# Performance work log

Hardware: AMD Instinct MI355X
Metric: run time of the kernel (lower is better)

The kernel has to match this reference:

```python
import jax, jax.numpy as jnp
import numpy as np
from jax import lax

L, B, D = 512, 128, 512   # listener frames, batch, listener feature dim
T, E, C, H, V = 200, 384, 128, 512, 46  # decode steps, embed, context, hidden(=E+C), vocab


def setup_inputs() -> dict:
    key = jax.random.key(0)
    ks = jax.random.split(key, 32)
    def p(i, shape, s=0.02):
        return jax.random.normal(ks[i], shape, dtype=jnp.float32) * s
    return {
        "listener_features": jax.random.normal(ks[0], (L, B, D), dtype=jnp.float32),
        "utterance_lengths": jax.random.randint(ks[1], (B,), L // 2, L + 1),
        "transcript": jax.random.randint(ks[2], (T, B), 0, V),
        "embedding": p(3, (V, E), 1.0),
        "w_ih0": p(4, (4 * H, E + C)), "w_hh0": p(5, (4 * H, H)),
        "b_ih0": jnp.zeros((4 * H,), jnp.float32), "b_hh0": jnp.zeros((4 * H,), jnp.float32),
        "w_ih1": p(6, (4 * H, H)), "w_hh1": p(7, (4 * H, H)),
        "b_ih1": jnp.zeros((4 * H,), jnp.float32), "b_hh1": jnp.zeros((4 * H,), jnp.float32),
        "w_ih2": p(8, (4 * H, H)), "w_hh2": p(9, (4 * H, H)),
        "b_ih2": jnp.zeros((4 * H,), jnp.float32), "b_hh2": jnp.zeros((4 * H,), jnp.float32),
        "phi_w": p(10, (C, H)), "phi_b": jnp.zeros((C,), jnp.float32),
        "key_w": p(11, (C, D)), "key_b": jnp.zeros((C,), jnp.float32),
        "value_w": p(12, (C, D)), "value_b": jnp.zeros((C,), jnp.float32),
        "out_w": p(13, (V, H + C)), "out_b": jnp.zeros((V,), jnp.float32),
        "init_hx0": jnp.zeros((1, H), jnp.float32), "init_cx0": jnp.zeros((1, H), jnp.float32),
        "init_hx1": jnp.zeros((1, H), jnp.float32), "init_cx1": jnp.zeros((1, H), jnp.float32),
        "init_hx2": jnp.zeros((1, H), jnp.float32), "init_cx2": jnp.zeros((1, H), jnp.float32),
    }


def _lstm_cell(x, h, c, w_ih, w_hh, b_ih, b_hh):
    gates = x @ w_ih.T + b_ih + h @ w_hh.T + b_hh  # [B,4H]
    i, f, g, o = jnp.split(gates, 4, axis=-1)
    c2 = jax.nn.sigmoid(f) * c + jax.nn.sigmoid(i) * jnp.tanh(g)
    h2 = jax.nn.sigmoid(o) * jnp.tanh(c2)
    return h2, c2


def reference(listener_features, utterance_lengths, transcript, embedding,
              w_ih0, w_hh0, b_ih0, b_hh0, w_ih1, w_hh1, b_ih1, b_hh1,
              w_ih2, w_hh2, b_ih2, b_hh2, phi_w, phi_b, key_w, key_b,
              value_w, value_b, out_w, out_b,
              init_hx0, init_cx0, init_hx1, init_cx1, init_hx2, init_cx2):
    nL, nB = listener_features.shape[0], listener_features.shape[1]
    mask = (jnp.arange(nL)[None, :] < utterance_lengths[:, None]).astype(jnp.float32)  # [B,L]
    # key/value projections are step-invariant (original recomputes them each step; same math)
    keyf = jnp.einsum('lbd,cd->blc', listener_features, key_w) + key_b   # [B,L,C]
    valf = jnp.einsum('lbd,cd->blc', listener_features, value_w) + value_b  # [B,L,C]

    def attend(hx2):
        q = hx2 @ phi_w.T + phi_b                      # [B,C]
        energy = jnp.einsum('bc,blc->bl', q, keyf)     # [B,L]
        a = jax.nn.softmax(energy, axis=-1) * mask
        a = a / jnp.maximum(jnp.sum(a, axis=-1, keepdims=True), 1e-12)  # F.normalize(p=1)
        ctx = jnp.einsum('bl,blc->bc', a, valf)        # [B,C]
        return a, ctx

    hx0 = jnp.broadcast_to(init_hx0, (nB, H)); cx0 = jnp.broadcast_to(init_cx0, (nB, H))
    hx1 = jnp.broadcast_to(init_hx1, (nB, H)); cx1 = jnp.broadcast_to(init_cx1, (nB, H))
    hx2 = jnp.broadcast_to(init_hx2, (nB, H)); cx2 = jnp.broadcast_to(init_cx2, (nB, H))
    _, ctx = attend(hx2)  # initial context from initial decoder state

    # teacher forcing: step t consumes <sos>(=0) then transcript[t-1]
    in_chars = jnp.concatenate([jnp.zeros((1, nB), transcript.dtype), transcript[:-1]], axis=0)  # [T,B]
    emb = embedding[in_chars]  # [T,B,E]

    def step(carry, emb_t):
        hx0, cx0, hx1, cx1, hx2, cx2, ctx = carry
        x = jnp.concatenate([emb_t, ctx], axis=-1)  # [B,E+C]
        hx0, cx0 = _lstm_cell(x, hx0, cx0, w_ih0, w_hh0, b_ih0, b_hh0)
        hx1, cx1 = _lstm_cell(hx0, hx1, cx1, w_ih1, w_hh1, b_ih1, b_hh1)
        hx2, cx2 = _lstm_cell(hx1, hx2, cx2, w_ih2, w_hh2, b_ih2, b_hh2)
        a, ctx = attend(hx2)
        logits = jnp.concatenate([hx2, ctx], axis=-1) @ out_w.T + out_b  # [B,V]
        return (hx0, cx0, hx1, cx1, hx2, cx2, ctx), (logits, a)

    carry0 = (hx0, cx0, hx1, cx1, hx2, cx2, ctx)
    _, (logits, attn) = lax.scan(step, carry0, emb)
    return logits, attn  # [T,B,V], [T,B,L]
```

## Files before the change

### kernel.cpp

```cpp
#include <hip/hip_runtime.h>

typedef unsigned short UST;
typedef unsigned int uint32;
typedef float f32x4 __attribute__((ext_vector_type(4)));
typedef short s16x8 __attribute__((ext_vector_type(8)));


__device__ __forceinline__ float b2f(UST u) {
  uint32 x = ((uint32)u) << 16;
  union { uint32 u; float f; } v; v.u = x; return v.f;
}
__device__ __forceinline__ UST f2bf(float f) {
  union { float f; uint32 u; } v; v.f = f;
  uint32 r = (v.u + 0x7fffu + ((v.u >> 16) & 1u)) >> 16;
  return (UST)r;
}
__device__ __forceinline__ ushort4 f2bf4(float4 v) {
  ushort4 r; r.x = f2bf(v.x); r.y = f2bf(v.y); r.z = f2bf(v.z); r.w = f2bf(v.w); return r;
}
__device__ __forceinline__ float sigf(float x) { return 1.f / (1.f + __expf(-x)); }
__device__ __forceinline__ float tanhf_(float x) { return 2.f / (1.f + __expf(-2.f * x)) - 1.f; }

union U8 { unsigned long long u; ushort4 s; uint2 w; };
union UU16 { uint4 u; s16x8 v; };

__device__ __forceinline__ void st_flag(int* p, int v) {
  __hip_atomic_store(p, v, __ATOMIC_RELAXED, __HIP_MEMORY_SCOPE_AGENT);
}
__device__ __forceinline__ int ld_flag(const int* p) {
  return __hip_atomic_load(p, __ATOMIC_RELAXED, __HIP_MEMORY_SCOPE_AGENT);
}
__device__ __forceinline__ unsigned long long ld8(const void* p) {
  return __hip_atomic_load((const unsigned long long*)p, __ATOMIC_RELAXED, __HIP_MEMORY_SCOPE_AGENT);
}
__device__ __forceinline__ void st4(void* p, uint32 v) {
  __hip_atomic_store((uint32*)p, v, __ATOMIC_RELAXED, __HIP_MEMORY_SCOPE_AGENT);
}
__device__ __forceinline__ uint4 ld16c(const UST* p) {
  U8 a, b; a.u = ld8(p); b.u = ld8(p + 4);
  uint4 v; v.x = a.w.x; v.y = a.w.y; v.z = b.w.x; v.w = b.w.y; return v;
}

__device__ __forceinline__ void signal_flag(int* fl, int idx, int val, int tid) {
  __atomic_signal_fence(__ATOMIC_SEQ_CST);
  __builtin_amdgcn_s_waitcnt(0);
  __atomic_signal_fence(__ATOMIC_SEQ_CST);
  __syncthreads();
  if (tid == 0) st_flag(&fl[idx * 16], val);
}
__device__ __forceinline__ void wait128f(int* fl, int val, int tid, unsigned long long dl) {
  if (tid < 128) {
    while (ld_flag(&fl[tid * 16]) < val) {
      if (__builtin_amdgcn_s_memrealtime() > dl) break;
      __builtin_amdgcn_s_sleep(1);
    }
  }
  __syncthreads();
}
template <int SPW>
__device__ __forceinline__ void poll_cols(int w, int qd, int* fl, int val,
                                          unsigned long long dl) {
  int base = (w * SPW) * 4 + qd;
  for (;;) {
    bool ok = true;
#pragma unroll
    for (int j = 0; j < SPW; ++j)
      ok &= (ld_flag(&fl[(base + j * 4) * 16]) >= val);
    if (ok) break;
    if (__builtin_amdgcn_s_memrealtime() > dl) break;
    __builtin_amdgcn_s_sleep(1);
  }
}
__device__ __forceinline__ void poll_rows(int ln, int* fl, int val, unsigned long long dl) {
  for (;;) {
    bool ok = true;
#pragma unroll
    for (int rt = 0; rt < 4; ++rt)
      ok &= (ld_flag(&fl[(rt * 16 + ln) * 16]) >= val);
    if (ok) break;
    if (__builtin_amdgcn_s_memrealtime() > dl) break;
    __builtin_amdgcn_s_sleep(1);
  }
}

struct Args {
  const float* lf; const int* ulen; const int* tr; const float* emb;
  const float* wih0; const float* whh0; const float* bih0; const float* bhh0;
  const float* wih1; const float* whh1; const float* bih1; const float* bhh1;
  const float* wih2; const float* whh2; const float* bih2; const float* bhh2;
  const float* phi_w; const float* phi_b; const float* key_w; const float* key_b;
  const float* val_w; const float* val_b; const float* out_w; const float* out_b;
  const float* ihx0; const float* icx0; const float* ihx1; const float* icx1;
  const float* ihx2; const float* icx2;
  int* bar; UST* wr; UST* xemb; UST* phi_bf; UST* keyfT; UST* valfT;
  UST* hx0; UST* hx1; UST* hx2; UST* ctx; UST* h2h; UST* cxh;
  float* out_logits; float* out_attn;
};

__global__ void __launch_bounds__(256) kprep(Args A) {
  const long N0 = 8192;
  const long N1 = 3L * 2048 * 1024;
  const long N2 = 200L * 128 * 384;
  const long N3 = 128L * 512;
  long total = N0 + N1 + N2 + N3;
  long stride = (long)gridDim.x * blockDim.x;
  for (long ii = (long)blockIdx.x * 256 + threadIdx.x; ii < total; ii += stride) {
    long j = ii;
    if (j < N0) { A.bar[j] = 0; continue; }
    j -= N0;
    if (j < N1) {
      int q = (int)j;
      int i = q & 7, lane = (q >> 3) & 63, nt = (q >> 9) & 1, ks = (q >> 10) & 31;
      int js = (q >> 15) & 63, cell = q >> 21;
      int gr = js * 32 + nt * 16 + (lane & 15);
      int jc = gr >> 2, g = gr & 3, k = ks * 32 + (lane >> 4) * 8 + i;
      const float* wi = cell == 0 ? A.wih0 : cell == 1 ? A.wih1 : A.wih2;
      const float* wh = cell == 0 ? A.whh0 : cell == 1 ? A.whh1 : A.whh2;
      float v;
      if (cell == 0)
        v = (k < 384) ? wi[(g * 512 + jc) * 512 + k]
          : (k < 896) ? wh[(g * 512 + jc) * 512 + k - 384]
                      : wi[(g * 512 + jc) * 512 + k - 512];
      else
        v = (k < 512) ? wi[(g * 512 + jc) * 512 + k] : wh[(g * 512 + jc) * 512 + k - 512];
      A.wr[j] = f2bf(v);
      continue;
    }
    j -= N1;
    if (j < N2) {
      int t = (int)(j / 49152); int r = (int)(j % 49152); int bb = r / 384; int e = r - bb * 384;
      int ch = (t == 0) ? 0 : A.tr[(t - 1) * 128 + bb];
      A.xemb[j] = f2bf(A.emb[ch * 384 + e]);
      continue;
    }
    j -= N2;
    A.phi_bf[j] = f2bf(A.phi_w[j]);
  }
}

__global__ void __launch_bounds__(256) kkv(Args A) {
  __shared__ __attribute__((aligned(16))) char sm[17408 + 34816];
  UST (*A_lds)[136] = (UST(*)[136])sm;
  UST (*W_lds)[136] = (UST(*)[136])(sm + 17408);
  float* sbuf = (float*)(sm + 17408);
  int tid = threadIdx.x, lane = tid & 63, wv = tid >> 6, ln = lane & 15, qd = lane >> 4;
  int blk = blockIdx.x;
  int b = blk >> 4, lt = (blk >> 1) & 7, kv = blk & 1;
  int l0 = lt * 64;
  const float* W = kv ? A.val_w : A.key_w;
  const float* bs = kv ? A.val_b : A.key_b;
  UST* outp = kv ? A.valfT : A.keyfT;
  f32x4 acc[8];
#pragma unroll
  for (int nt = 0; nt < 8; ++nt) {
    float x = bs[nt * 16 + ln];
    f32x4 t; t[0] = x; t[1] = x; t[2] = x; t[3] = x; acc[nt] = t;
  }
  for (int cc = 0; cc < 4; ++cc) {
    int d0 = cc * 128;
#pragma unroll
    for (int it = 0; it < 8; ++it) {
      int idx = it * 256 + tid, row = idx >> 5, seg = idx & 31;
      float4 v = *(const float4*)(A.lf + ((size_t)(l0 + row) * 128 + b) * 512 + d0 + seg * 4);
      *(ushort4*)&A_lds[row][seg * 4] = f2bf4(v);
    }
#pragma unroll
    for (int it = 0; it < 16; ++it) {
      int idx = it * 256 + tid, row = idx >> 5, seg = idx & 31;
      float4 v = *(const float4*)(W + (size_t)row * 512 + d0 + seg * 4);
      *(ushort4*)&W_lds[row][seg * 4] = f2bf4(v);
    }
    __syncthreads();
#pragma unroll
    for (int ks = 0; ks < 4; ++ks) {
      s16x8 av = *(const s16x8*)&A_lds[wv * 16 + ln][ks * 32 + qd * 8];
#pragma unroll
      for (int nt = 0; nt < 8; ++nt) {
        s16x8 bv = *(const s16x8*)&W_lds[nt * 16 + ln][ks * 32 + qd * 8];
        acc[nt] = __builtin_amdgcn_mfma_f32_16x16x32_bf16(av, bv, acc[nt], 0, 0, 0);
      }
    }
    __syncthreads();
  }
#pragma unroll
  for (int nt = 0; nt < 8; ++nt)
#pragma unroll
    for (int r = 0; r < 4; ++r)
      sbuf[(wv * 16 + qd * 4 + r) * 128 + nt * 16 + ln] = acc[nt][r];
  __syncthreads();
  int c2 = tid >> 1, lh = tid & 1;
  for (int g8 = 0; g8 < 4; ++g8) {
    UST tmp[8];
#pragma unroll
    for (int i = 0; i < 8; ++i) tmp[i] = f2bf(sbuf[(lh * 32 + g8 * 8 + i) * 128 + c2]);
    *(uint4*)(outp + ((size_t)b * 128 + c2) * 512 + l0 + lh * 32 + g8 * 8) = *(uint4*)tmp;
  }
}

template <int SPW>
__device__ __forceinline__ void load_c(int w, int ln, int qd, const UST* src, int rowStride,
                                       int colOff, s16x8 af[4][4]) {
#pragma unroll
  for (int j = 0; j < SPW; ++j) {
    int c = (w * SPW + j) * 4 + qd + colOff;
#pragma unroll
    for (int rt = 0; rt < 4; ++rt) {
      UU16 u; u.u = ld16c(src + (rt * 16 + ln) * rowStride + c * 8);
      af[j][rt] = u.v;
    }
  }
}
template <int SPW>
__device__ __forceinline__ void compute_d(int w, int ln, int qd, int lane,
    const UST* wb, int ksgBase, const s16x8 af[4][4], f32x4 acc[4][2]) {
#pragma unroll
  for (int j = 0; j < SPW; ++j) {
    int ksg = ksgBase + w * SPW + j;
    s16x8 b0 = *(const s16x8*)(wb + ((size_t)(ksg * 2 + 0) * 64 + lane) * 8);
    s16x8 b1 = *(const s16x8*)(wb + ((size_t)(ksg * 2 + 1) * 64 + lane) * 8);
#pragma unroll
    for (int rt = 0; rt < 4; ++rt) {
      acc[rt][0] = __builtin_amdgcn_mfma_f32_16x16x32_bf16(af[j][rt], b0, acc[rt][0], 0, 0, 0);
      acc[rt][1] = __builtin_amdgcn_mfma_f32_16x16x32_bf16(af[j][rt], b1, acc[rt][1], 0, 0, 0);
    }
  }
}
__device__ __forceinline__ void zacc(f32x4 acc[4][2]) {
#pragma unroll
  for (int rt = 0; rt < 4; ++rt)
#pragma unroll
    for (int nt = 0; nt < 2; ++nt) {
      acc[rt][nt][0] = 0.f; acc[rt][nt][1] = 0.f; acc[rt][nt][2] = 0.f; acc[rt][nt][3] = 0.f;
    }
}
__device__ __forceinline__ void cell_epilogue(const Args& A, int cell, int t, int m, int j0,
    int tid, int w, int ln, int qd, f32x4 acc[4][2], float* FB,
    const float* bias8, float* cr, UST* hdst) {
  __syncthreads();
#pragma unroll
  for (int rt = 0; rt < 4; ++rt)
#pragma unroll
    for (int nt = 0; nt < 2; ++nt)
#pragma unroll
      for (int reg = 0; reg < 4; ++reg)
        FB[w * 2112 + (rt * 16 + qd * 4 + reg) * 33 + nt * 16 + ln] = acc[rt][nt][reg];
  __syncthreads();
  int row = tid >> 2, q4 = tid & 3, grow = m * 64 + row;
  uint32 upack = 0;
#pragma unroll
  for (int jj = 0; jj < 2; ++jj) {
    int gc = (q4 * 2 + jj) * 4;
    int o = row * 33 + gc;
    float g0 = FB[o] + FB[2112 + o] + FB[4224 + o] + FB[6336 + o] + bias8[jj * 4 + 0];
    float g1 = FB[o + 1] + FB[2112 + o + 1] + FB[4224 + o + 1] + FB[6336 + o + 1] + bias8[jj * 4 + 1];
    float g2 = FB[o + 2] + FB[2112 + o + 2] + FB[4224 + o + 2] + FB[6336 + o + 2] + bias8[jj * 4 + 2];
    float g3 = FB[o + 3] + FB[2112 + o + 3] + FB[4224 + o + 3] + FB[6336 + o + 3] + bias8[jj * 4 + 3];
    float cn = sigf(g1) * cr[jj] + sigf(g0) * tanhf_(g2);
    float hv = sigf(g3) * tanhf_(cn);
    cr[jj] = cn;
    upack |= ((uint32)f2bf(hv)) << (16 * jj);
  }
  st4(hdst + grow * 512 + j0 + q4 * 2, upack);
  if (cell == 2) *(uint32*)(A.h2h + ((size_t)t * 128 + grow) * 512 + j0 + q4 * 2) = upack;
}

__device__ __forceinline__ void attend_f(const Args& A, int t, int p, int b, int tid,
    int lane, int wv, char* smraw, const uint4 (&rgK)[32], const uint4 (&rgV)[32],
    int* pf, int pv, unsigned long long dl) {
  float* att_h = (float*)smraw;
  float* att_q = att_h + 512;
  float* att_c = att_q + 256;
  float* att_red = att_c + 128;
  float (*e_part)[512] = (float(*)[512])(att_red + 16);
  const UST* hx2p = A.hx2 + p * 65536;
  if (tid < 128) {
    const int* fp = &pf[(tid >> 1) * 16];
    while (ld_flag(fp) < pv) {
      if (__builtin_amdgcn_s_memrealtime() > dl) break;
      __builtin_amdgcn_s_sleep(1);
    }
    U8 v; v.u = ld8(hx2p + b * 512 + tid * 4);
    att_h[tid * 4 + 0] = b2f(v.s.x); att_h[tid * 4 + 1] = b2f(v.s.y);
    att_h[tid * 4 + 2] = b2f(v.s.z); att_h[tid * 4 + 3] = b2f(v.s.w);
  }
  __syncthreads();
  int c = tid & 127, half = tid >> 7;
  {
    float acc = half ? 0.f : A.phi_b[c];
    const UST* pr = A.phi_bf + c * 512 + half * 256;
    const float* hh = att_h + half * 256;
#pragma unroll 4
    for (int k = 0; k < 256; k += 8) {
      uint4 v = *(const uint4*)(pr + k);
      const UST* us = (const UST*)&v;
#pragma unroll
      for (int i = 0; i < 8; ++i) acc += b2f(us[i]) * hh[k + i];
    }
    att_q[tid] = acc;
  }
  __syncthreads();
  if (tid < 128) att_q[tid] += att_q[tid + 128];
  __syncthreads();
  {
    int cg = tid >> 6, lg = tid & 63;
    float ep[8] = {0, 0, 0, 0, 0, 0, 0, 0};
#pragma unroll
    for (int i = 0; i < 32; ++i) {
      float qv = att_q[cg * 32 + i];
      const UST* us = (const UST*)&rgK[i];
#pragma unroll
      for (int j = 0; j < 8; ++j) ep[j] += qv * b2f(us[j]);
    }
#pragma unroll
    for (int i = 0; i < 8; ++i) e_part[cg][lg * 8 + i] = ep[i];
  }
  __syncthreads();
  float e0 = e_part[0][2 * tid] + e_part[1][2 * tid] + e_part[2][2 * tid] + e_part[3][2 * tid];
  float e1 = e_part[0][2 * tid + 1] + e_part[1][2 * tid + 1] + e_part[2][2 * tid + 1] + e_part[3][2 * tid + 1];
  float mx = fmaxf(e0, e1);
#pragma unroll
  for (int off = 32; off; off >>= 1) mx = fmaxf(mx, __shfl_xor(mx, off));
  if (lane == 0) att_red[wv] = mx;
  __syncthreads();
  mx = fmaxf(fmaxf(att_red[0], att_red[1]), fmaxf(att_red[2], att_red[3]));
  int len = A.ulen[b];
  float x0 = (2 * tid < len) ? __expf(e0 - mx) : 0.f;
  float x1 = (2 * tid + 1 < len) ? __expf(e1 - mx) : 0.f;
  float s = x0 + x1;
#pragma unroll
  for (int off = 32; off; off >>= 1) s += __shfl_xor(s, off);
  if (lane == 0) att_red[8 + wv] = s;
  __syncthreads();
  s = att_red[8] + att_red[9] + att_red[10] + att_red[11];
  float inv = 1.f / fmaxf(s, 1e-12f);
  float a0 = x0 * inv, a1 = x1 * inv;
  float* esm = &e_part[0][0];
  esm[2 * tid] = a0; esm[2 * tid + 1] = a1;
  if (t >= 0) {
    float2 st; st.x = a0; st.y = a1;
    *(float2*)(A.out_attn + ((size_t)t * 128 + b) * 512 + 2 * tid) = st;
  }
  __syncthreads();
  {
    float acc = 0.f;
    const float* aa = esm + half * 256;
#pragma unroll
    for (int i = 0; i < 32; ++i) {
      const UST* us = (const UST*)&rgV[i];
#pragma unroll
      for (int j = 0; j < 8; ++j) acc += aa[i * 8 + j] * b2f(us[j]);
    }
    att_q[tid] = acc;
  }
  __syncthreads();
  if (tid < 128) att_c[tid] = att_q[tid] + att_q[tid + 128];
  __syncthreads();
  if (tid < 64) {
    float cv0 = att_c[2 * tid], cv1 = att_c[2 * tid + 1];
    uint32 u = (uint32)f2bf(cv0) | ((uint32)f2bf(cv1) << 16);
    st4(A.ctx + p * 16384 + b * 128 + 2 * tid, u);
    if (t >= 0) *(uint32*)(A.cxh + ((size_t)t * 128 + b) * 128 + 2 * tid) = u;
  }
}

__global__ void __launch_bounds__(256, 1) kmain(Args A) {
  __shared__ __attribute__((aligned(16))) char smraw[65536];
  unsigned long long dl = __builtin_amdgcn_s_memrealtime() + 100000000ull;
  int blk = blockIdx.x, tid = threadIdx.x;
  int lane = tid & 63, w = tid >> 6, ln = lane & 15, qd = lane >> 4;
  int* c0f = A.bar;
  int* c1f = A.bar + 2048;
  int* c2f = A.bar + 4096;
  int* attf = A.bar + 6144;
  if (blk < 128) {
    float* FB = (float*)smraw;
    int js = ((blk >> 4) << 3) | (blk & 7);
    int m = (blk >> 3) & 1;
    int j0 = js * 8;
    int sid = m * 64 + js;
    int* mc0 = c0f + m * 1024;
    int* mc1 = c1f + m * 1024;
    int* mc2 = c2f + m * 1024;
    int* mat = attf + m * 1024;
    float bias[3][8]; float cr[3][2];
    {
      const float* bihA[3] = {A.bih0, A.bih1, A.bih2};
      const float* bhhA[3] = {A.bhh0, A.bhh1, A.bhh2};
      const float* icxA[3] = {A.icx0, A.icx1, A.icx2};
      const float* ihxA[3] = {A.ihx0, A.ihx1, A.ihx2};
      UST* hxA[3] = {A.hx0, A.hx1, A.hx2};
      int q4 = tid & 3;
#pragma unroll
      for (int cI = 0; cI < 3; ++cI) {
#pragma unroll
        for (int jj = 0; jj < 2; ++jj) {
          int col = j0 + q4 * 2 + jj;
          for (int g = 0; g < 4; ++g)
            bias[cI][jj * 4 + g] = bihA[cI][g * 512 + col] + bhhA[cI][g * 512 + col];
          cr[cI][jj] = icxA[cI][col];
        }
        int row = tid >> 2, grow = m * 64 + row, col0 = j0 + q4 * 2;
        uint32 u = (uint32)f2bf(ihxA[cI][col0]) | ((uint32)f2bf(ihxA[cI][col0 + 1]) << 16);
        st4(hxA[cI] + 65536 + grow * 512 + col0, u);
      }
    }
    signal_flag(c2f, sid, 1, tid);
    wait128f(c2f, 1, tid, dl);
    const UST* wrj0 = A.wr + (size_t)js * 32768;
    const UST* wrj1 = wrj0 + 2097152;
    const UST* wrj2 = wrj0 + 4194304;
    f32x4 acc0[4][2], acc1[4][2], acc2[4][2];
    s16x8 af[4][4];
    for (int t = 0; t < 200; ++t) {
      int p = t & 1, po = p ^ 1;
      const UST* xe = A.xemb + (size_t)t * 49152 + m * 64 * 384;
      const UST* h0r = A.hx0 + po * 65536 + m * 64 * 512;
      const UST* h1r = A.hx1 + po * 65536 + m * 64 * 512;
      const UST* h2r = A.hx2 + po * 65536 + m * 64 * 512;
      const UST* cxr = A.ctx + po * 16384 + m * 64 * 128;
      zacc(acc0); zacc(acc1); zacc(acc2);
      if (w < 3) {
#pragma unroll
        for (int j = 0; j < 4; ++j) {
          int cc = (w * 4 + j) * 4 + qd;
#pragma unroll
          for (int rt = 0; rt < 4; ++rt) {
            UU16 u; u.u = *(const uint4*)(xe + (rt * 16 + ln) * 384 + cc * 8);
            af[j][rt] = u.v;
          }
        }
      } else {
        load_c<4>(w, ln, qd, h0r, 512, -48, af);
      }
      compute_d<4>(w, ln, qd, lane, wrj0, 0, af, acc0);
      load_c<3>(w, ln, qd, h0r, 512, 16, af);
      compute_d<3>(w, ln, qd, lane, wrj0, 16, af, acc0);
      load_c<4>(w, ln, qd, h1r, 512, 0, af);
      compute_d<4>(w, ln, qd, lane, wrj1, 16, af, acc1);
      poll_cols<4>(w, qd, mc2, t + 1, dl);
      load_c<4>(w, ln, qd, h2r, 512, 0, af);
      compute_d<4>(w, ln, qd, lane, wrj2, 16, af, acc2);
      poll_rows(ln, mat, t + 1, dl);
      {
        int cc = w * 4 + qd;
#pragma unroll
        for (int rt = 0; rt < 4; ++rt) {
          UU16 u; u.u = ld16c(cxr + (rt * 16 + ln) * 128 + cc * 8);
          af[0][rt] = u.v;
        }
      }
      compute_d<1>(w, ln, qd, lane, wrj0, 28, af, acc0);
      cell_epilogue(A, 0, t, m, j0, tid, w, ln, qd, acc0, FB, bias[0], cr[0], A.hx0 + p * 65536);
      signal_flag(c0f, sid, t + 2, tid);
      const UST* h0n = A.hx0 + p * 65536 + m * 64 * 512;
      poll_cols<4>(w, qd, mc0, t + 2, dl);
      load_c<4>(w, ln, qd, h0n, 512, 0, af);
      compute_d<4>(w, ln, qd, lane, wrj1, 0, af, acc1);
      cell_epilogue(A, 1, t, m, j0, tid, w, ln, qd, acc1, FB, bias[1], cr[1], A.hx1 + p * 65536);
      signal_flag(c1f, sid, t + 2, tid);
      const UST* h1n = A.hx1 + p * 65536 + m * 64 * 512;
      poll_cols<4>(w, qd, mc1, t + 2, dl);
      load_c<4>(w, ln, qd, h1n, 512, 0, af);
      compute_d<4>(w, ln, qd, lane, wrj2, 0, af, acc2);
      cell_epilogue(A, 2, t, m, j0, tid, w, ln, qd, acc2, FB, bias[2], cr[2], A.hx2 + p * 65536);
      signal_flag(c2f, sid, t + 2, tid);
    }
  } else {
    int b = blk - 128;
    int* mc2a = c2f + (b >> 6) * 1024;
    uint4 rgK[32], rgV[32];
    {
      int cg = tid >> 6, lg = tid & 63;
      const UST* kb = A.keyfT + (size_t)b * 65536 + lg * 8;
#pragma unroll
      for (int i = 0; i < 32; ++i)
        rgK[i] = *(const uint4*)(kb + (size_t)(cg * 32 + i) * 512);
      int c = tid & 127, half = tid >> 7;
      const UST* vb = A.valfT + (size_t)b * 65536 + (size_t)c * 512 + half * 256;
#pragma unroll
      for (int i = 0; i < 32; ++i)
        rgV[i] = *(const uint4*)(vb + i * 8);
    }
    attend_f(A, -1, 1, b, tid, lane, w, smraw, rgK, rgV, mc2a, 1, dl);
    signal_flag(attf, b, 1, tid);
    for (int t = 0; t < 200; ++t) {
      attend_f(A, t, t & 1, b, tid, lane, w, smraw, rgK, rgV, mc2a, t + 2, dl);
      signal_flag(attf, b, t + 2, tid);
    }
  }
}

__global__ void __launch_bounds__(256) kepi(Args A) {
  __shared__ UST ow[46 * 648];
  __shared__ float ob[46];
  int t = blockIdx.x, tid = threadIdx.x;
  for (int i = tid; i < 46 * 640; i += 256) {
    int v = i / 640, k = i - v * 640; ow[v * 648 + k] = f2bf(A.out_w[i]);
  }
  if (tid < 46) ob[tid] = A.out_b[tid];
  __syncthreads();
  for (int oi = tid; oi < 128 * 46; oi += 256) {
    int bb = oi / 46, v = oi - bb * 46;
    const UST* xh = A.h2h + ((size_t)t * 128 + bb) * 512;
    const UST* xc = A.cxh + ((size_t)t * 128 + bb) * 128;
    const UST* wrow = &ow[v * 648];
    float acc = ob[v];
    for (int k = 0; k < 512; k += 8) {
      uint4 xv = *(const uint4*)(xh + k);
      uint4 wv4 = *(const uint4*)(wrow + k);
      const UST* xs = (const UST*)&xv; const UST* wl = (const UST*)&wv4;
#pragma unroll
      for (int i = 0; i < 8; ++i) acc += b2f(xs[i]) * b2f(wl[i]);
    }
    for (int k = 0; k < 128; k += 8) {
      uint4 xv = *(const uint4*)(xc + k);
      uint4 wv4 = *(const uint4*)(wrow + 512 + k);
      const UST* xs = (const UST*)&xv; const UST* wl = (const UST*)&wv4;
#pragma unroll
      for (int i = 0; i < 8; ++i) acc += b2f(xs[i]) * b2f(wl[i]);
    }
    A.out_logits[((size_t)t * 128 + bb) * 46 + v] = acc;
  }
}

extern "C" void kernel_launch(void* const* d_in, const int* in_sizes, int n_in,
                              void* d_out, int out_size, void* d_ws, size_t ws_size,
                              hipStream_t stream) {
  (void)in_sizes; (void)n_in; (void)out_size; (void)ws_size;
  Args a;
  a.lf = (const float*)d_in[0]; a.ulen = (const int*)d_in[1]; a.tr = (const int*)d_in[2];
  a.emb = (const float*)d_in[3];
  a.wih0 = (const float*)d_in[4]; a.whh0 = (const float*)d_in[5]; a.bih0 = (const float*)d_in[6]; a.bhh0 = (const float*)d_in[7];
  a.wih1 = (const float*)d_in[8]; a.whh1 = (const float*)d_in[9]; a.bih1 = (const float*)d_in[10]; a.bhh1 = (const float*)d_in[11];
  a.wih2 = (const float*)d_in[12]; a.whh2 = (const float*)d_in[13]; a.bih2 = (const float*)d_in[14]; a.bhh2 = (const float*)d_in[15];
  a.phi_w = (const float*)d_in[16]; a.phi_b = (const float*)d_in[17];
  a.key_w = (const float*)d_in[18]; a.key_b = (const float*)d_in[19];
  a.val_w = (const float*)d_in[20]; a.val_b = (const float*)d_in[21];
  a.out_w = (const float*)d_in[22]; a.out_b = (const float*)d_in[23];
  a.ihx0 = (const float*)d_in[24]; a.icx0 = (const float*)d_in[25];
  a.ihx1 = (const float*)d_in[26]; a.icx1 = (const float*)d_in[27];
  a.ihx2 = (const float*)d_in[28]; a.icx2 = (const float*)d_in[29];
  char* ws = (char*)d_ws;
  a.bar    = (int*)ws;
  a.wr     = (UST*)(ws + 32768);
  a.xemb   = (UST*)(ws + 12615680);
  a.phi_bf = (UST*)(ws + 32276480);
  a.keyfT  = (UST*)(ws + 32407552);
  a.valfT  = (UST*)(ws + 49184768);
  a.hx0    = (UST*)(ws + 65961984);
  a.hx1    = (UST*)(ws + 66224128);
  a.hx2    = (UST*)(ws + 66486272);
  a.ctx    = (UST*)(ws + 66748416);
  a.h2h    = (UST*)(ws + 66813952);
  a.cxh    = (UST*)(ws + 93028352);
  a.out_logits = (float*)d_out;
  a.out_attn   = (float*)d_out + 1177600;
  kprep<<<4096, 256, 0, stream>>>(a);
  kkv<<<2048, 256, 0, stream>>>(a);
  kmain<<<256, 256, 0, stream>>>(a);
  kepi<<<200, 256, 0, stream>>>(a);
}
```

Measured before the change: 7.558 ms.

## Switch LSTM blocks to per-wave row bands with per-wave flags and LDS staging

```diff
diff --git a/kernel.cpp b/kernel.cpp
--- a/kernel.cpp
+++ b/kernel.cpp
@@ -22,7 +22,6 @@
 __device__ __forceinline__ float tanhf_(float x) { return 2.f / (1.f + __expf(-2.f * x)) - 1.f; }
 
 union U8 { unsigned long long u; ushort4 s; uint2 w; };
-union UU16 { uint4 u; s16x8 v; };
 
 __device__ __forceinline__ void st_flag(int* p, int v) {
   __hip_atomic_store(p, v, __ATOMIC_RELAXED, __HIP_MEMORY_SCOPE_AGENT);
@@ -30,15 +29,57 @@
 __device__ __forceinline__ int ld_flag(const int* p) {
   return __hip_atomic_load(p, __ATOMIC_RELAXED, __HIP_MEMORY_SCOPE_AGENT);
 }
-__device__ __forceinline__ unsigned long long ld8(const void* p) {
-  return __hip_atomic_load((const unsigned long long*)p, __ATOMIC_RELAXED, __HIP_MEMORY_SCOPE_AGENT);
-}
 __device__ __forceinline__ void st4(void* p, uint32 v) {
   __hip_atomic_store((uint32*)p, v, __ATOMIC_RELAXED, __HIP_MEMORY_SCOPE_AGENT);
 }
-__device__ __forceinline__ uint4 ld16c(const UST* p) {
-  U8 a, b; a.u = ld8(p); b.u = ld8(p + 4);
-  uint4 v; v.x = a.w.x; v.y = a.w.y; v.z = b.w.x; v.w = b.w.y; return v;
+
+__device__ __forceinline__ void ld16x_h(const UST* p0, uint4 rg[16]) {
+  const UST* p1 = p0 + 4 * 512;
+  const UST* p2 = p0 + 8 * 512;
+  const UST* p3 = p0 + 12 * 512;
+  asm volatile(
+    "global_load_dwordx4 %0, %16, off sc1\n\t"
+    "global_load_dwordx4 %1, %16, off offset:1024 sc1\n\t"
+    "global_load_dwordx4 %2, %16, off offset:2048 sc1\n\t"
+    "global_load_dwordx4 %3, %16, off offset:3072 sc1\n\t"
+    "global_load_dwordx4 %4, %17, off sc1\n\t"
+    "global_load_dwordx4 %5, %17, off offset:1024 sc1\n\t"
+    "global_load_dwordx4 %6, %17, off offset:2048 sc1\n\t"
+    "global_load_dwordx4 %7, %17, off offset:3072 sc1\n\t"
+    "global_load_dwordx4 %8, %18, off sc1\n\t"
+    "global_load_dwordx4 %9, %18, off offset:1024 sc1\n\t"
+    "global_load_dwordx4 %10, %18, off offset:2048 sc1\n\t"
+    "global_load_dwordx4 %11, %18, off offset:3072 sc1\n\t"
+    "global_load_dwordx4 %12, %19, off sc1\n\t"
+    "global_load_dwordx4 %13, %19, off offset:1024 sc1\n\t"
+    "global_load_dwordx4 %14, %19, off offset:2048 sc1\n\t"
+    "global_load_dwordx4 %15, %19, off offset:3072 sc1\n\t"
+    "s_waitcnt vmcnt(0)"
+    : "=&v"(rg[0]), "=&v"(rg[1]), "=&v"(rg[2]), "=&v"(rg[3]),
+      "=&v"(rg[4]), "=&v"(rg[5]), "=&v"(rg[6]), "=&v"(rg[7]),
+      "=&v"(rg[8]), "=&v"(rg[9]), "=&v"(rg[10]), "=&v"(rg[11]),
+      "=&v"(rg[12]), "=&v"(rg[13]), "=&v"(rg[14]), "=&v"(rg[15])
+    : "v"(p0), "v"(p1), "v"(p2), "v"(p3)
+    : "memory");
+}
+__device__ __forceinline__ void ld4x_ctx(const UST* p0, uint4 rg[4]) {
+  asm volatile(
+    "global_load_dwordx4 %0, %4, off sc1\n\t"
+    "global_load_dwordx4 %1, %4, off offset:256 sc1\n\t"
+    "global_load_dwordx4 %2, %4, off offset:512 sc1\n\t"
+    "global_load_dwordx4 %3, %4, off offset:768 sc1\n\t"
+    "s_waitcnt vmcnt(0)"
+    : "=&v"(rg[0]), "=&v"(rg[1]), "=&v"(rg[2]), "=&v"(rg[3])
+    : "v"(p0) : "memory");
+}
+__device__ __forceinline__ uint2 ld2c(const UST* p) {
+  uint2 r;
+  asm volatile("global_load_dwordx2 %0, %1, off sc1\n\ts_waitcnt vmcnt(0)"
+               : "=&v"(r) : "v"(p) : "memory");
+  return r;
+}
+__device__ __forceinline__ void lgkm0() {
+  asm volatile("s_waitcnt lgkmcnt(0)" ::: "memory");
 }
 
 __device__ __forceinline__ void signal_flag(int* fl, int idx, int val, int tid) {
@@ -57,27 +98,10 @@
   }
   __syncthreads();
 }
-template <int SPW>
-__device__ __forceinline__ void poll_cols(int w, int qd, int* fl, int val,
-                                          unsigned long long dl) {
-  int base = (w * SPW) * 4 + qd;
-  for (;;) {
-    bool ok = true;
-#pragma unroll
-    for (int j = 0; j < SPW; ++j)
-      ok &= (ld_flag(&fl[(base + j * 4) * 16]) >= val);
-    if (ok) break;
-    if (__builtin_amdgcn_s_memrealtime() > dl) break;
-    __builtin_amdgcn_s_sleep(1);
-  }
-}
-__device__ __forceinline__ void poll_rows(int ln, int* fl, int val, unsigned long long dl) {
-  for (;;) {
-    bool ok = true;
-#pragma unroll
-    for (int rt = 0; rt < 4; ++rt)
-      ok &= (ld_flag(&fl[(rt * 16 + ln) * 16]) >= val);
-    if (ok) break;
+__device__ __forceinline__ void pollw(int* arr, int m64, int w, int val, int lane,
+                                      unsigned long long dl) {
+  const int* fp = &arr[((m64 + lane) * 4 + w) * 16];
+  while (ld_flag(fp) < val) {
     if (__builtin_amdgcn_s_memrealtime() > dl) break;
     __builtin_amdgcn_s_sleep(1);
   }
@@ -98,7 +122,7 @@
 };
 
 __global__ void __launch_bounds__(256) kprep(Args A) {
-  const long N0 = 8192;
+  const long N0 = 32768;
   const long N1 = 3L * 2048 * 1024;
   const long N2 = 200L * 128 * 384;
   const long N3 = 128L * 512;
@@ -197,76 +221,65 @@
   }
 }
 
-template <int SPW>
-__device__ __forceinline__ void load_c(int w, int ln, int qd, const UST* src, int rowStride,
-                                       int colOff, s16x8 af[4][4]) {
-#pragma unroll
-  for (int j = 0; j < SPW; ++j) {
-    int c = (w * SPW + j) * 4 + qd + colOff;
-#pragma unroll
-    for (int rt = 0; rt < 4; ++rt) {
-      UU16 u; u.u = ld16c(src + (rt * 16 + ln) * rowStride + c * 8);
-      af[j][rt] = u.v;
-    }
-  }
-}
-template <int SPW>
-__device__ __forceinline__ void compute_d(int w, int ln, int qd, int lane,
-    const UST* wb, int ksgBase, const s16x8 af[4][4], f32x4 acc[4][2]) {
-#pragma unroll
-  for (int j = 0; j < SPW; ++j) {
-    int ksg = ksgBase + w * SPW + j;
+__device__ __forceinline__ void bandwr(char* band, int lane, const uint4 rg[16]) {
+#pragma unroll
+  for (int r = 0; r < 16; ++r)
+    *(uint4*)(band + r * 1024 + (lane ^ (r & 7)) * 16) = rg[r];
+}
+template <int NK>
+__device__ __forceinline__ void comp_band(const char* band, int ln, int qd, int lane,
+    const UST* wb, int ksgBase, f32x4 acc[2]) {
+#pragma unroll
+  for (int k = 0; k < NK; ++k) {
+    int ksg = ksgBase + k;
+    int cb = k * 4 + qd;
+    s16x8 a = *(const s16x8*)(band + ln * 1024 + ((cb ^ (ln & 7))) * 16);
     s16x8 b0 = *(const s16x8*)(wb + ((size_t)(ksg * 2 + 0) * 64 + lane) * 8);
     s16x8 b1 = *(const s16x8*)(wb + ((size_t)(ksg * 2 + 1) * 64 + lane) * 8);
-#pragma unroll
-    for (int rt = 0; rt < 4; ++rt) {
-      acc[rt][0] = __builtin_amdgcn_mfma_f32_16x16x32_bf16(af[j][rt], b0, acc[rt][0], 0, 0, 0);
-      acc[rt][1] = __builtin_amdgcn_mfma_f32_16x16x32_bf16(af[j][rt], b1, acc[rt][1], 0, 0, 0);
-    }
-  }
-}
-__device__ __forceinline__ void zacc(f32x4 acc[4][2]) {
-#pragma unroll
-  for (int rt = 0; rt < 4; ++rt)
-#pragma unroll
-    for (int nt = 0; nt < 2; ++nt) {
-      acc[rt][nt][0] = 0.f; acc[rt][nt][1] = 0.f; acc[rt][nt][2] = 0.f; acc[rt][nt][3] = 0.f;
-    }
-}
-__device__ __forceinline__ void cell_epilogue(const Args& A, int cell, int t, int m, int j0,
-    int tid, int w, int ln, int qd, f32x4 acc[4][2], float* FB,
-    const float* bias8, float* cr, UST* hdst) {
-  __syncthreads();
-#pragma unroll
-  for (int rt = 0; rt < 4; ++rt)
-#pragma unroll
-    for (int nt = 0; nt < 2; ++nt)
-#pragma unroll
-      for (int reg = 0; reg < 4; ++reg)
-        FB[w * 2112 + (rt * 16 + qd * 4 + reg) * 33 + nt * 16 + ln] = acc[rt][nt][reg];
-  __syncthreads();
-  int row = tid >> 2, q4 = tid & 3, grow = m * 64 + row;
-  uint32 upack = 0;
-#pragma unroll
-  for (int jj = 0; jj < 2; ++jj) {
-    int gc = (q4 * 2 + jj) * 4;
-    int o = row * 33 + gc;
-    float g0 = FB[o] + FB[2112 + o] + FB[4224 + o] + FB[6336 + o] + bias8[jj * 4 + 0];
-    float g1 = FB[o + 1] + FB[2112 + o + 1] + FB[4224 + o + 1] + FB[6336 + o + 1] + bias8[jj * 4 + 1];
-    float g2 = FB[o + 2] + FB[2112 + o + 2] + FB[4224 + o + 2] + FB[6336 + o + 2] + bias8[jj * 4 + 2];
-    float g3 = FB[o + 3] + FB[2112 + o + 3] + FB[4224 + o + 3] + FB[6336 + o + 3] + bias8[jj * 4 + 3];
-    float cn = sigf(g1) * cr[jj] + sigf(g0) * tanhf_(g2);
-    float hv = sigf(g3) * tanhf_(cn);
-    cr[jj] = cn;
-    upack |= ((uint32)f2bf(hv)) << (16 * jj);
-  }
-  st4(hdst + grow * 512 + j0 + q4 * 2, upack);
-  if (cell == 2) *(uint32*)(A.h2h + ((size_t)t * 128 + grow) * 512 + j0 + q4 * 2) = upack;
+    acc[0] = __builtin_amdgcn_mfma_f32_16x16x32_bf16(a, b0, acc[0], 0, 0, 0);
+    acc[1] = __builtin_amdgcn_mfma_f32_16x16x32_bf16(a, b1, acc[1], 0, 0, 0);
+  }
+}
+__device__ __forceinline__ void zacc2(f32x4 a[2]) {
+  a[0][0]=0.f; a[0][1]=0.f; a[0][2]=0.f; a[0][3]=0.f;
+  a[1][0]=0.f; a[1][1]=0.f; a[1][2]=0.f; a[1][3]=0.f;
+}
+__device__ __forceinline__ void epi_wave(const Args& A, int cell, int t, int m64, int w16,
+    int lane, int ln, int qd, int j0, f32x4 acc[2], const float biasL[2], float (*cr)[4],
+    char* band, UST* hdst, int* flg, int fv) {
+#pragma unroll
+  for (int nt = 0; nt < 2; ++nt) {
+#pragma unroll
+    for (int reg = 0; reg < 4; ++reg) {
+      float v = acc[nt][reg] + biasL[nt];
+      float s1 = __shfl_xor(v, 1);
+      float s2 = __shfl_xor(v, 2);
+      float s3 = __shfl_xor(s1, 2);
+      float cn = sigf(s1) * cr[nt][reg] + sigf(v) * tanhf_(s2);
+      float hv = sigf(s3) * tanhf_(cn);
+      cr[nt][reg] = cn;
+      if ((ln & 3) == 0)
+        *(UST*)(band + (qd * 4 + reg) * 16 + (nt * 4 + (ln >> 2)) * 2) = f2bf(hv);
+    }
+  }
+  lgkm0();
+  if (lane < 16) {
+    uint4 hh = *(const uint4*)(band + lane * 16);
+    int grow = m64 + w16 + lane;
+    UST* d = hdst + (size_t)grow * 512 + j0;
+    st4(d + 0, hh.x); st4(d + 2, hh.y); st4(d + 4, hh.z); st4(d + 6, hh.w);
+    if (cell == 2)
+      *(uint4*)(A.h2h + ((size_t)t * 128 + grow) * 512 + j0) = hh;
+  }
+  __atomic_signal_fence(__ATOMIC_SEQ_CST);
+  __builtin_amdgcn_s_waitcnt(0);
+  __atomic_signal_fence(__ATOMIC_SEQ_CST);
+  if (lane == 0) st_flag(flg, fv);
 }
 
 __device__ __forceinline__ void attend_f(const Args& A, int t, int p, int b, int tid,
     int lane, int wv, char* smraw, const uint4 (&rgK)[32], const uint4 (&rgV)[32],
-    int* pf, int pv, unsigned long long dl) {
+    const int* fp, int pv, unsigned long long dl) {
   float* att_h = (float*)smraw;
   float* att_q = att_h + 512;
   float* att_c = att_q + 256;
@@ -274,12 +287,11 @@
   float (*e_part)[512] = (float(*)[512])(att_red + 16);
   const UST* hx2p = A.hx2 + p * 65536;
   if (tid < 128) {
-    const int* fp = &pf[(tid >> 1) * 16];
     while (ld_flag(fp) < pv) {
       if (__builtin_amdgcn_s_memrealtime() > dl) break;
       __builtin_amdgcn_s_sleep(1);
     }
-    U8 v; v.u = ld8(hx2p + b * 512 + tid * 4);
+    U8 v; v.w = ld2c(hx2p + b * 512 + tid * 4);
     att_h[tid * 4 + 0] = b2f(v.s.x); att_h[tid * 4 + 1] = b2f(v.s.y);
     att_h[tid * 4 + 2] = b2f(v.s.z); att_h[tid * 4 + 3] = b2f(v.s.w);
   }
@@ -368,106 +380,134 @@
   unsigned long long dl = __builtin_amdgcn_s_memrealtime() + 100000000ull;
   int blk = blockIdx.x, tid = threadIdx.x;
   int lane = tid & 63, w = tid >> 6, ln = lane & 15, qd = lane >> 4;
-  int* c0f = A.bar;
-  int* c1f = A.bar + 2048;
-  int* c2f = A.bar + 4096;
-  int* attf = A.bar + 6144;
+  int* c0f4 = A.bar;
+  int* c1f4 = A.bar + 8192;
+  int* c2f4 = A.bar + 16384;
+  int* attf = A.bar + 24576;
+  int* initf = A.bar + 26624;
   if (blk < 128) {
-    float* FB = (float*)smraw;
+    char* band = smraw + w * 16384;
     int js = ((blk >> 4) << 3) | (blk & 7);
     int m = (blk >> 3) & 1;
     int j0 = js * 8;
     int sid = m * 64 + js;
-    int* mc0 = c0f + m * 1024;
-    int* mc1 = c1f + m * 1024;
-    int* mc2 = c2f + m * 1024;
-    int* mat = attf + m * 1024;
-    float bias[3][8]; float cr[3][2];
+    int m64 = m * 64;
+    int w16 = w * 16;
+    float biasL[3][2]; float cr[3][2][4];
     {
       const float* bihA[3] = {A.bih0, A.bih1, A.bih2};
       const float* bhhA[3] = {A.bhh0, A.bhh1, A.bhh2};
       const float* icxA[3] = {A.icx0, A.icx1, A.icx2};
       const float* ihxA[3] = {A.ihx0, A.ihx1, A.ihx2};
       UST* hxA[3] = {A.hx0, A.hx1, A.hx2};
-      int q4 = tid & 3;
+      int gL = ln & 3, jcl = ln >> 2;
 #pragma unroll
       for (int cI = 0; cI < 3; ++cI) {
 #pragma unroll
-        for (int jj = 0; jj < 2; ++jj) {
-          int col = j0 + q4 * 2 + jj;
-          for (int g = 0; g < 4; ++g)
-            bias[cI][jj * 4 + g] = bihA[cI][g * 512 + col] + bhhA[cI][g * 512 + col];
-          cr[cI][jj] = icxA[cI][col];
+        for (int nt = 0; nt < 2; ++nt) {
+          int col = j0 + nt * 4 + jcl;
+          biasL[cI][nt] = bihA[cI][gL * 512 + col] + bhhA[cI][gL * 512 + col];
+#pragma unroll
+          for (int reg = 0; reg < 4; ++reg) cr[cI][nt][reg] = icxA[cI][col];
         }
-        int row = tid >> 2, grow = m * 64 + row, col0 = j0 + q4 * 2;
+        int row = tid >> 2, grow = m64 + row, q4 = tid & 3, col0 = j0 + q4 * 2;
         uint32 u = (uint32)f2bf(ihxA[cI][col0]) | ((uint32)f2bf(ihxA[cI][col0 + 1]) << 16);
         st4(hxA[cI] + 65536 + grow * 512 + col0, u);
       }
     }
-    signal_flag(c2f, sid, 1, tid);
-    wait128f(c2f, 1, tid, dl);
+    signal_flag(initf, sid, 1, tid);
+    wait128f(initf, 1, tid, dl);
+    if (lane == 0) {
+      st_flag(&c0f4[(sid * 4 + w) * 16], 1);
+      st_flag(&c1f4[(sid * 4 + w) * 16], 1);
+      st_flag(&c2f4[(sid * 4 + w) * 16], 1);
+    }
     const UST* wrj0 = A.wr + (size_t)js * 32768;
     const UST* wrj1 = wrj0 + 2097152;
     const UST* wrj2 = wrj0 + 4194304;
-    f32x4 acc0[4][2], acc1[4][2], acc2[4][2];
-    s16x8 af[4][4];
+    int* myc0 = &c0f4[(sid * 4 + w) * 16];
+    int* myc1 = &c1f4[(sid * 4 + w) * 16];
+    int* myc2 = &c2f4[(sid * 4 + w) * 16];
     for (int t = 0; t < 200; ++t) {
       int p = t & 1, po = p ^ 1;
-      const UST* xe = A.xemb + (size_t)t * 49152 + m * 64 * 384;
-      const UST* h0r = A.hx0 + po * 65536 + m * 64 * 512;
-      const UST* h1r = A.hx1 + po * 65536 + m * 64 * 512;
-      const UST* h2r = A.hx2 + po * 65536 + m * 64 * 512;
-      const UST* cxr = A.ctx + po * 16384 + m * 64 * 128;
-      zacc(acc0); zacc(acc1); zacc(acc2);
-      if (w < 3) {
-#pragma unroll
-        for (int j = 0; j < 4; ++j) {
-          int cc = (w * 4 + j) * 4 + qd;
-#pragma unroll
-          for (int rt = 0; rt < 4; ++rt) {
-            UU16 u; u.u = *(const uint4*)(xe + (rt * 16 + ln) * 384 + cc * 8);
-            af[j][rt] = u.v;
-          }
+      const UST* xe = A.xemb + (size_t)t * 49152 + m64 * 384;
+      const UST* h0r = A.hx0 + po * 65536 + m64 * 512;
+      const UST* h1r = A.hx1 + po * 65536 + m64 * 512;
+      const UST* h2r = A.hx2 + po * 65536 + m64 * 512;
+      const UST* cxr = A.ctx + po * 16384 + m64 * 128;
+      f32x4 acc0[2], acc1[2], acc2[2];
+      zacc2(acc0); zacc2(acc1); zacc2(acc2);
+      {
+        uint4 rg[16];
+        if (lane < 48) {
+#pragma unroll
+          for (int r = 0; r < 16; ++r)
+            rg[r] = *(const uint4*)(xe + (size_t)(w16 + r) * 384 + lane * 8);
+        } else {
+          ld16x_h(h0r + (size_t)w16 * 512 + (lane - 48) * 8, rg);
         }
-      } else {
-        load_c<4>(w, ln, qd, h0r, 512, -48, af);
+        bandwr(band, lane, rg);
       }
-      compute_d<4>(w, ln, qd, lane, wrj0, 0, af, acc0);
-      load_c<3>(w, ln, qd, h0r, 512, 16, af);
-      compute_d<3>(w, ln, qd, lane, wrj0, 16, af, acc0);
-      load_c<4>(w, ln, qd, h1r, 512, 0, af);
-      compute_d<4>(w, ln, qd, lane, wrj1, 16, af, acc1);
-      poll_cols<4>(w, qd, mc2, t + 1, dl);
-      load_c<4>(w, ln, qd, h2r, 512, 0, af);
-      compute_d<4>(w, ln, qd, lane, wrj2, 16, af, acc2);
-      poll_rows(ln, mat, t + 1, dl);
+      lgkm0();
+      comp_band<16>(band, ln, qd, lane, wrj0, 0, acc0);
       {
-        int cc = w * 4 + qd;
-#pragma unroll
-        for (int rt = 0; rt < 4; ++rt) {
-          UU16 u; u.u = ld16c(cxr + (rt * 16 + ln) * 128 + cc * 8);
-          af[0][rt] = u.v;
+        uint4 rg[16];
+        if (lane < 48) {
+          ld16x_h(h0r + (size_t)w16 * 512 + (lane + 16) * 8, rg);
+          bandwr(band, lane, rg);
         }
       }
-      compute_d<1>(w, ln, qd, lane, wrj0, 28, af, acc0);
-      cell_epilogue(A, 0, t, m, j0, tid, w, ln, qd, acc0, FB, bias[0], cr[0], A.hx0 + p * 65536);
-      signal_flag(c0f, sid, t + 2, tid);
-      const UST* h0n = A.hx0 + p * 65536 + m * 64 * 512;
-      poll_cols<4>(w, qd, mc0, t + 2, dl);
-      load_c<4>(w, ln, qd, h0n, 512, 0, af);
-      compute_d<4>(w, ln, qd, lane, wrj1, 0, af, acc1);
-      cell_epilogue(A, 1, t, m, j0, tid, w, ln, qd, acc1, FB, bias[1], cr[1], A.hx1 + p * 65536);
-      signal_flag(c1f, sid, t + 2, tid);
-      const UST* h1n = A.hx1 + p * 65536 + m * 64 * 512;
-      poll_cols<4>(w, qd, mc1, t + 2, dl);
-      load_c<4>(w, ln, qd, h1n, 512, 0, af);
-      compute_d<4>(w, ln, qd, lane, wrj2, 0, af, acc2);
-      cell_epilogue(A, 2, t, m, j0, tid, w, ln, qd, acc2, FB, bias[2], cr[2], A.hx2 + p * 65536);
-      signal_flag(c2f, sid, t + 2, tid);
+      lgkm0();
+      comp_band<12>(band, ln, qd, lane, wrj0, 16, acc0);
+      { uint4 rg[16]; ld16x_h(h1r + (size_t)w16 * 512 + lane * 8, rg); bandwr(band, lane, rg); }
+      lgkm0();
+      comp_band<16>(band, ln, qd, lane, wrj1, 16, acc1);
+      pollw(c2f4, m64, w, t + 1, lane, dl);
+      { uint4 rg[16]; ld16x_h(h2r + (size_t)w16 * 512 + lane * 8, rg); bandwr(band, lane, rg); }
+      lgkm0();
+      comp_band<16>(band, ln, qd, lane, wrj2, 16, acc2);
+      {
+        int cc = lane & 15, rq = lane >> 4;
+        for (;;) {
+          bool ok = true;
+#pragma unroll
+          for (int rr = 0; rr < 4; ++rr)
+            ok &= (ld_flag(&attf[(m64 + w16 + rq * 4 + rr) * 16]) >= t + 1);
+          if (ok) break;
+          if (__builtin_amdgcn_s_memrealtime() > dl) break;
+          __builtin_amdgcn_s_sleep(1);
+        }
+        uint4 rg4[4];
+        ld4x_ctx(cxr + (size_t)(w16 + rq * 4) * 128 + cc * 8, rg4);
+#pragma unroll
+        for (int rr = 0; rr < 4; ++rr) {
+          int r = rq * 4 + rr;
+          *(uint4*)(band + r * 1024 + ((cc ^ (r & 7))) * 16) = rg4[rr];
+        }
+      }
+      lgkm0();
+      comp_band<4>(band, ln, qd, lane, wrj0, 28, acc0);
+      epi_wave(A, 0, t, m64, w16, lane, ln, qd, j0, acc0, biasL[0], cr[0], band,
+               A.hx0 + p * 65536, myc0, t + 2);
+      pollw(c0f4, m64, w, t + 2, lane, dl);
+      const UST* h0n = A.hx0 + p * 65536 + m64 * 512;
+      { uint4 rg[16]; ld16x_h(h0n + (size_t)w16 * 512 + lane * 8, rg); bandwr(band, lane, rg); }
+      lgkm0();
+      comp_band<16>(band, ln, qd, lane, wrj1, 0, acc1);
+      epi_wave(A, 1, t, m64, w16, lane, ln, qd, j0, acc1, biasL[1], cr[1], band,
+               A.hx1 + p * 65536, myc1, t + 2);
+      pollw(c1f4, m64, w, t + 2, lane, dl);
+      const UST* h1n = A.hx1 + p * 65536 + m64 * 512;
+      { uint4 rg[16]; ld16x_h(h1n + (size_t)w16 * 512 + lane * 8, rg); bandwr(band, lane, rg); }
+      lgkm0();
+      comp_band<16>(band, ln, qd, lane, wrj2, 0, acc2);
+      epi_wave(A, 2, t, m64, w16, lane, ln, qd, j0, acc2, biasL[2], cr[2], band,
+               A.hx2 + p * 65536, myc2, t + 2);
     }
   } else {
     int b = blk - 128;
-    int* mc2a = c2f + (b >> 6) * 1024;
+    int m = b >> 6, wb = (b & 63) >> 4;
+    const int* myf = &c2f4[(((m * 64) + (tid >> 1)) * 4 + wb) * 16];
     uint4 rgK[32], rgV[32];
     {
       int cg = tid >> 6, lg = tid & 63;
@@ -481,10 +521,11 @@
       for (int i = 0; i < 32; ++i)
         rgV[i] = *(const uint4*)(vb + i * 8);
     }
-    attend_f(A, -1, 1, b, tid, lane, w, smraw, rgK, rgV, mc2a, 1, dl);
+    wait128f(initf, 1, tid, dl);
+    attend_f(A, -1, 1, b, tid, lane, w, smraw, rgK, rgV, myf, 1, dl);
     signal_flag(attf, b, 1, tid);
     for (int t = 0; t < 200; ++t) {
-      attend_f(A, t, t & 1, b, tid, lane, w, smraw, rgK, rgV, mc2a, t + 2, dl);
+      attend_f(A, t, t & 1, b, tid, lane, w, smraw, rgK, rgV, myf, t + 2, dl);
       signal_flag(attf, b, t + 2, tid);
     }
   }
@@ -542,17 +583,17 @@
   a.ihx2 = (const float*)d_in[28]; a.icx2 = (const float*)d_in[29];
   char* ws = (char*)d_ws;
   a.bar    = (int*)ws;
-  a.wr     = (UST*)(ws + 32768);
-  a.xemb   = (UST*)(ws + 12615680);
-  a.phi_bf = (UST*)(ws + 32276480);
-  a.keyfT  = (UST*)(ws + 32407552);
-  a.valfT  = (UST*)(ws + 49184768);
-  a.hx0    = (UST*)(ws + 65961984);
-  a.hx1    = (UST*)(ws + 66224128);
-  a.hx2    = (UST*)(ws + 66486272);
-  a.ctx    = (UST*)(ws + 66748416);
-  a.h2h    = (UST*)(ws + 66813952);
-  a.cxh    = (UST*)(ws + 93028352);
+  a.wr     = (UST*)(ws + 131072);
+  a.xemb   = (UST*)(ws + 12713984);
+  a.phi_bf = (UST*)(ws + 32374784);
+  a.keyfT  = (UST*)(ws + 32505856);
+  a.valfT  = (UST*)(ws + 49283072);
+  a.hx0    = (UST*)(ws + 66060288);
+  a.hx1    = (UST*)(ws + 66322432);
+  a.hx2    = (UST*)(ws + 66584576);
+  a.ctx    = (UST*)(ws + 66846720);
+  a.h2h    = (UST*)(ws + 66912256);
+  a.cxh    = (UST*)(ws + 93126656);
   a.out_logits = (float*)d_out;
   a.out_attn   = (float*)d_out + 1177600;
   kprep<<<4096, 256, 0, stream>>>(a);
```

Measured after the change: 8.985 ms. +18.9%, slower.
